# Performance work log

Hardware: AMD Instinct MI355X
Metric: run time of the kernel (lower is better)

The kernel has to match this reference:

```python
import jax, jax.numpy as jnp
import numpy as np

HEADS = 8
DK = 64   # key_size (defaults to size_per_head)
DV = 64   # size_per_head
RATE = 4
OUT = HEADS * DV  # 512


def extract_seq_patches(x, kernel, rate):
    # x: [b, L, d] -> [b, L, kernel, d]; strided local window gather
    b, L, d = x.shape
    k_size = kernel + (rate - 1) * (kernel - 1)
    p_right = (k_size - 1) // 2
    p_left = k_size - 1 - p_right
    xp = jnp.pad(x, ((0, 0), (p_left, p_right), (0, 0)))
    patches = [xp[:, i:i + L] for i in range(0, k_size, rate)]  # kernel slices
    return jnp.stack(patches, axis=2)


def setup_inputs() -> dict:
    key = jax.random.key(0)
    k1, k2, k3, k4 = jax.random.split(key, 4)
    s = 1.0 / np.sqrt(OUT)
    x = jax.random.normal(k1, (2, 4096, OUT), dtype=jnp.float32)
    Wq = jax.random.normal(k2, (OUT, HEADS * DK), dtype=jnp.float32) * s
    Wk = jax.random.normal(k3, (OUT, HEADS * DK), dtype=jnp.float32) * s
    Wv = jax.random.normal(k4, (OUT, HEADS * DV), dtype=jnp.float32) * s
    return {"x": x, "Wq": Wq, "Wk": Wk, "Wv": Wv}


def reference(x, Wq, Wk, Wv):
    b, L, d = x.shape
    pad = RATE - L % RATE  # torch code always pads (pad=RATE when L % RATE == 0)
    xpad = jnp.pad(x, ((0, 0), (0, pad), (0, 0)))
    nL = L + pad
    n = nL // RATE
    kernel = 2 * RATE - 1  # 1 + 2*neighbors

    qw = xpad @ Wq
    kw = xpad @ Wk
    vw = xpad @ Wv

    kwp = extract_seq_patches(kw, kernel, RATE)  # [b, nL, K, H*dk]
    vwp = extract_seq_patches(vw, kernel, RATE)  # [b, nL, K, H*dv]

    # [b, h, r, n, d]
    qw = qw.reshape(b, n, RATE, HEADS, DK).transpose(0, 3, 2, 1, 4)
    kw = kw.reshape(b, n, RATE, HEADS, DK).transpose(0, 3, 2, 1, 4)
    vw = vw.reshape(b, n, RATE, HEADS, DV).transpose(0, 3, 2, 1, 4)
    # [b, h, r, n, K, d]
    kwp = kwp.reshape(b, n, RATE, kernel, HEADS, DK).transpose(0, 4, 2, 1, 3, 5)
    vwp = vwp.reshape(b, n, RATE, kernel, HEADS, DV).transpose(0, 4, 2, 1, 3, 5)

    scale = 1.0 / np.sqrt(DK)
    a = jnp.einsum('bhrnd,bhrmd->bhrnm', qw, kw) * scale    # strided scores [b,h,r,n,n]
    ap = jnp.einsum('bhrnd,bhrnkd->bhrnk', qw, kwp) * scale  # local scores  [b,h,r,n,K]

    A = jax.nn.softmax(jnp.concatenate([a, ap], axis=-1), axis=-1)
    a, ap = A[..., :n], A[..., n:]

    o = jnp.einsum('bhrnm,bhrmd->bhrnd', a, vw) + jnp.einsum('bhrnk,bhrnkd->bhrnd', ap, vwp)
    o = o.transpose(0, 3, 2, 1, 4).reshape(b, nL, HEADS * DV)
    return o[:, :L]
```

## Files before the change

### kernel.cpp

```cpp
#include <hip/hip_runtime.h>
#include <hip/hip_bf16.h>


#define BATCH 2
#define LSEQ  4096
#define DMODEL 512
#define NH    8
#define DHEAD 64
#define NPAD  1088
#define QSCALE 0.18033688011112042f

typedef __bf16 bf16x8 __attribute__((ext_vector_type(8)));
typedef __attribute__((ext_vector_type(4))) float f32x4;
typedef __attribute__((ext_vector_type(16))) float f32x16;
typedef unsigned short u16;
typedef unsigned int u32;
typedef __attribute__((ext_vector_type(8))) u16 u16x8;
typedef __attribute__((ext_vector_type(4))) u16 u16x4;
typedef __attribute__((ext_vector_type(4))) u32 u32x4;

__device__ __forceinline__ u16 f2bf(float f) {
    u32 u = __float_as_uint(f);
    u += 0x7fffu + ((u >> 16) & 1u);
    return (u16)(u >> 16);
}

__device__ __forceinline__ u32 cvtpk(float lo, float hi) {
    u32 d;
    asm("v_cvt_pk_bf16_f32 %0, %1, %2" : "=v"(d) : "v"(lo), "v"(hi));
    return d;
}

__device__ __forceinline__ void gload16(const u16* g, u16* l) {
    __builtin_amdgcn_global_load_lds(
        (const __attribute__((address_space(1))) u32*)(const void*)g,
        (__attribute__((address_space(3))) u32*)(void*)l, 16, 0, 0);
}

__device__ __forceinline__ f32x16 zero16() {
    f32x16 v;
    #pragma unroll
    for (int i = 0; i < 16; ++i) v[i] = 0.f;
    return v;
}

__global__ __launch_bounds__(256) void prep_kernel(
    const float* __restrict__ x,
    const float* __restrict__ Wq, const float* __restrict__ Wk, const float* __restrict__ Wv,
    u16* __restrict__ xb, u16* __restrict__ Wt)
{
    const int bid = blockIdx.x, tid = threadIdx.x;
    if (bid < 2048) {
        const size_t i0 = (size_t)bid * 2048 + (size_t)tid * 8;
        float4 a = *(const float4*)(x + i0);
        float4 b = *(const float4*)(x + i0 + 4);
        u16x8 o = { f2bf(a.x), f2bf(a.y), f2bf(a.z), f2bf(a.w),
                    f2bf(b.x), f2bf(b.y), f2bf(b.z), f2bf(b.w) };
        *(u16x8*)(xb + i0) = o;
    } else {
        const int wb  = bid - 2048;
        const int mat = wb >> 6;
        const int t   = wb & 63;
        const int k0  = (t >> 3) * 64, c0 = (t & 7) * 64;
        const float* W = (mat == 0) ? Wq : (mat == 1) ? Wk : Wv;
        __shared__ u16 Ws[64][72];
        #pragma unroll
        for (int i = 0; i < 4; ++i) {
            const int chunk = i * 256 + tid;
            const int kr = chunk >> 4, c4 = (chunk & 15) * 4;
            float4 v = *(const float4*)(W + (size_t)(k0 + kr) * DMODEL + c0 + c4);
            u16x4 q = { f2bf(v.x), f2bf(v.y), f2bf(v.z), f2bf(v.w) };
            *(u16x4*)&Ws[kr][c4] = q;
        }
        __syncthreads();
        const int cc = tid >> 2, kq = (tid & 3) * 16;
        alignas(16) u16 tmp[16];
        #pragma unroll
        for (int kk = 0; kk < 16; ++kk) tmp[kk] = Ws[kq + kk][cc];
        u16* dst = Wt + (size_t)(mat * 512 + c0 + cc) * DMODEL + k0 + kq;
        *(u16x8*)dst       = *(const u16x8*)&tmp[0];
        *(u16x8*)(dst + 8) = *(const u16x8*)&tmp[8];
    }
}

__global__ __launch_bounds__(256) void gemm_kernel(
    const u16* __restrict__ xb, const u16* __restrict__ Wt,
    u16* __restrict__ Qb, u16* __restrict__ Kb, u16* __restrict__ Vb)
{
    const int bid = blockIdx.x;
    const int xcd = bid & 7;
    const int j   = bid >> 3;
    const int mt  = xcd * 8 + (j / 12);
    const int nt  = j % 12;
    const int m0 = mt * 128;
    const int n0 = nt * 128;
    const int tid = threadIdx.x;
    const int w = tid >> 6, l = tid & 63, lr = l & 15, lh = l >> 4;
    const int wr = w >> 1, wc = w & 1;

    __shared__ u16 smem[16896];
    u16* As = smem;
    u16* Bs = smem + 8192;

    f32x4 acc[4][4];
    const f32x4 fzero = {0.f, 0.f, 0.f, 0.f};
    #pragma unroll
    for (int mi = 0; mi < 4; ++mi)
        #pragma unroll
        for (int nj = 0; nj < 4; ++nj) acc[mi][nj] = fzero;

    for (int kt = 0; kt < 8; ++kt) {
        const int k0 = kt * 64;
        #pragma unroll
        for (int i = 0; i < 4; ++i) {
            const int cid = i * 256 + tid;
            const int row = cid >> 3, ch = cid & 7;
            const int sch = ch ^ (row & 7);
            u16* dstA = As + (i * 256 + w * 64) * 8;
            u16* dstB = Bs + (i * 256 + w * 64) * 8;
            gload16(xb + (size_t)(m0 + row) * DMODEL + k0 + sch * 8, dstA);
            gload16(Wt + (size_t)(n0 + row) * DMODEL + k0 + sch * 8, dstB);
        }
        __syncthreads();

        #pragma unroll
        for (int kk = 0; kk < 2; ++kk) {
            const int cs = (kk * 4 + lh) ^ (lr & 7);
            bf16x8 af[4], bfr[4];
            #pragma unroll
            for (int mi = 0; mi < 4; ++mi)
                af[mi] = *(const bf16x8*)(As + (wr * 64 + mi * 16 + lr) * 64 + cs * 8);
            #pragma unroll
            for (int nj = 0; nj < 4; ++nj)
                bfr[nj] = *(const bf16x8*)(Bs + (wc * 64 + nj * 16 + lr) * 64 + cs * 8);
            #pragma unroll
            for (int mi = 0; mi < 4; ++mi)
                #pragma unroll
                for (int nj = 0; nj < 4; ++nj)
                    acc[mi][nj] = __builtin_amdgcn_mfma_f32_16x16x32_bf16(af[mi], bfr[nj], acc[mi][nj], 0, 0, 0);
        }
        __syncthreads();
    }

    const int mat = nt >> 2;
    const int hp  = nt & 3;
    if (mat < 2) {
        u16* Ob = (mat == 0) ? Qb : Kb;
        const float osc = (mat == 0) ? QSCALE : 1.0f;
        #pragma unroll
        for (int mi = 0; mi < 4; ++mi) {
            const int gmb = m0 + wr * 64 + mi * 16 + lh * 4;
            const int b = gmb >> 12;
            #pragma unroll
            for (int rr = 0; rr < 4; ++rr) {
                const int t = (gmb + rr) & 4095;
                const int n = t >> 2, r = t & 3;
                #pragma unroll
                for (int nj = 0; nj < 4; ++nj) {
                    const int c  = wc * 64 + nj * 16 + lr;
                    const int h  = hp * 2 + (c >> 6);
                    const int dk = c & 63;
                    const size_t g = ((size_t)(b * NH + h)) * 4 + r;
                    Ob[(g * NPAD + n) * DHEAD + dk] = f2bf(acc[mi][nj][rr] * osc);
                }
            }
        }
    } else {
        #pragma unroll
        for (int mi = 0; mi < 4; ++mi) {
            const int nrel = wr * 16 + mi * 4 + lh;
            #pragma unroll
            for (int nj = 0; nj < 4; ++nj) {
                const int c = wc * 64 + nj * 16 + lr;
                #pragma unroll
                for (int rr = 0; rr < 4; ++rr)
                    smem[c * 132 + rr * 32 + nrel] = f2bf(acc[mi][nj][rr]);
            }
        }
        __syncthreads();
        const int b  = m0 >> 12;
        const int nb = (m0 & 4095) >> 2;
        #pragma unroll
        for (int e = 0; e < 2; ++e) {
            const int chunk = e * 256 + tid;
            const int c = chunk & 127, r = chunk >> 7;
            const int h  = hp * 2 + (c >> 6);
            const int dv = c & 63;
            const size_t g = ((size_t)(b * NH + h)) * 4 + r;
            u16* dst = Vb + (g * DHEAD + dv) * NPAD + nb;
            const u16* src = smem + c * 132 + r * 32;
            alignas(16) u16 tmp[32];
            #pragma unroll
            for (int q8 = 0; q8 < 8; ++q8)
                *(u16x4*)&tmp[q8 * 4] = *(const u16x4*)(src + q8 * 4);
            #pragma unroll
            for (int q16 = 0; q16 < 4; ++q16)
                *(u16x8*)(dst + q16 * 8) = *(const u16x8*)&tmp[q16 * 8];
        }
    }
}

__global__ __launch_bounds__(512, 4) void attn_kernel(
    const u16* __restrict__ Qb, const u16* __restrict__ Kb, const u16* __restrict__ Vb,
    float* __restrict__ out)
{
    const int g  = blockIdx.x;
    const int b  = g >> 5;
    const int h  = (g >> 2) & 7;
    const int r  = g & 3;
    const int q0 = blockIdx.y * 128;
    const int tid = threadIdx.x;
    const int w  = tid >> 6;
    const int wq = w & 3;
    const int kh = w >> 2;
    const int l  = tid & 63;
    const int lr = l & 31;
    const int hi = l >> 5;

    const u16* Qg  = Qb + (size_t)g * NPAD * DHEAD;
    const u16* Kg  = Kb + (size_t)g * NPAD * DHEAD;
    const u16* Vtg = Vb + (size_t)g * DHEAD * NPAD;

    __shared__ __align__(16) u16 KV[2][2][2][4096];
    float* red  = (float*)&KV[0][0][0][0];
    float* redL = red + 4 * 64 * 33;

    const int srow = tid >> 3;
    const int ssch = (tid & 7) ^ (srow & 7);
    const u16* ksrc0 = Kg  + (size_t)srow * DHEAD + ssch * 8;
    const u16* vsrc0 = Vtg + (size_t)srow * NPAD  + ssch * 8;

    bf16x8 qa[4];
    {
        const u16* qrow = Qg + (size_t)(q0 + wq * 32 + lr) * DHEAD + hi * 8;
        qa[0] = *(const bf16x8*)(qrow);
        qa[1] = *(const bf16x8*)(qrow + 16);
        qa[2] = *(const bf16x8*)(qrow + 32);
        qa[3] = *(const bf16x8*)(qrow + 48);
    }

    f32x16 o0 = zero16(), o1 = zero16();
    float Lown = 0.f;
    const int qw0 = q0 + wq * 32;
    const int qg  = qw0 + lr;

    gload16(ksrc0,                      &KV[0][0][0][w * 512]);
    gload16(ksrc0 + (size_t)512 * DHEAD, &KV[0][1][0][w * 512]);
    gload16(vsrc0,                      &KV[0][0][1][w * 512]);
    gload16(vsrc0 + 512,                &KV[0][1][1][w * 512]);

    for (int mt = 0; mt < 8; ++mt) {
        const int cur = mt & 1;
        if (mt < 7) {
            const size_t ko = (size_t)(mt + 1) * 64 * DHEAD;
            const int    vo = (mt + 1) * 64;
            gload16(ksrc0 + ko,                       &KV[cur ^ 1][0][0][w * 512]);
            gload16(ksrc0 + ko + (size_t)512 * DHEAD, &KV[cur ^ 1][1][0][w * 512]);
            gload16(vsrc0 + vo,                       &KV[cur ^ 1][0][1][w * 512]);
            gload16(vsrc0 + vo + 512,                 &KV[cur ^ 1][1][1][w * 512]);
            asm volatile("s_waitcnt vmcnt(4)" ::: "memory");
        } else {
            asm volatile("s_waitcnt vmcnt(0)" ::: "memory");
        }
        __builtin_amdgcn_s_barrier();

        const u16* Kbuf = &KV[cur][kh][0][0];
        const u16* Vbuf = &KV[cur][kh][1][0];

        f32x16 sA = zero16(), sB = zero16();
        __builtin_amdgcn_s_setprio(1);
        #pragma unroll
        for (int c = 0; c < 4; ++c) {
            const int slot = (c * 2 + hi) ^ (lr & 7);
            bf16x8 kbA = *(const bf16x8*)(Kbuf + (lr * 8 + slot) * 8);
            bf16x8 kbB = *(const bf16x8*)(Kbuf + ((32 + lr) * 8 + slot) * 8);
            sA = __builtin_amdgcn_mfma_f32_32x32x16_bf16(kbA, qa[c], sA, 0, 0, 0);
            sB = __builtin_amdgcn_mfma_f32_32x32x16_bf16(kbB, qa[c], sB, 0, 0, 0);
        }
        __builtin_amdgcn_s_setprio(0);

        const int mabs = kh * 512 + mt * 64;
        const bool special = (mabs + 66 >= qw0) && (mabs <= qw0 + 34);
        if (!special) {
            #pragma unroll
            for (int reg = 0; reg < 16; ++reg) {
                sA[reg] = __builtin_amdgcn_exp2f(sA[reg]);
                sB[reg] = __builtin_amdgcn_exp2f(sB[reg]);
                Lown += sA[reg] + sB[reg];
            }
        } else {
            #pragma unroll
            for (int reg = 0; reg < 16; ++reg) {
                const int krel = (reg & 3) + 8 * (reg >> 2) + 4 * hi;
                {
                    const int dd = mabs + krel - qg;
                    float v = sA[reg];
                    if (dd >= -3 && dd <= 3) v += 1.0f;
                    sA[reg] = __builtin_amdgcn_exp2f(v);
                }
                {
                    const int dd = mabs + 32 + krel - qg;
                    float v = sB[reg];
                    if (dd >= -3 && dd <= 3) v += 1.0f;
                    sB[reg] = __builtin_amdgcn_exp2f(v);
                }
                Lown += sA[reg] + sB[reg];
            }
        }

        u32 pkA[8], pkB[8];
        #pragma unroll
        for (int r2 = 0; r2 < 8; ++r2) {
            pkA[r2] = cvtpk(sA[2 * r2], sA[2 * r2 + 1]);
            pkB[r2] = cvtpk(sB[2 * r2], sB[2 * r2 + 1]);
        }

        __builtin_amdgcn_s_setprio(1);
        #pragma unroll
        for (int c = 0; c < 4; ++c) {
            const int c1 = c & 1;
            u32 p0, p1, p2, p3;
            if (c < 2) { p0 = pkA[4*c1]; p1 = pkA[4*c1+1]; p2 = pkA[4*c1+2]; p3 = pkA[4*c1+3]; }
            else       { p0 = pkB[4*c1]; p1 = pkB[4*c1+1]; p2 = pkB[4*c1+2]; p3 = pkB[4*c1+3]; }
            const u32 own0  = hi ? p2 : p0;
            const u32 own1  = hi ? p3 : p1;
            const u32 send0 = hi ? p0 : p2;
            const u32 send1 = hi ? p1 : p3;
            const u32 recv0 = (u32)__shfl_xor((int)send0, 32);
            const u32 recv1 = (u32)__shfl_xor((int)send1, 32);
            u32x4 paw;
            paw.x = hi ? recv0 : own0;
            paw.y = hi ? recv1 : own1;
            paw.z = hi ? own0  : recv0;
            paw.w = hi ? own1  : recv1;
            const bf16x8 pa = __builtin_bit_cast(bf16x8, paw);

            const int slot = (c * 2 + hi) ^ (lr & 7);
            bf16x8 vb0 = *(const bf16x8*)(Vbuf + (lr * 8 + slot) * 8);
            bf16x8 vb1 = *(const bf16x8*)(Vbuf + ((32 + lr) * 8 + slot) * 8);
            o0 = __builtin_amdgcn_mfma_f32_32x32x16_bf16(pa, vb0, o0, 0, 0, 0);
            o1 = __builtin_amdgcn_mfma_f32_32x32x16_bf16(pa, vb1, o1, 0, 0, 0);
        }
        __builtin_amdgcn_s_setprio(0);
        if (mt < 7) __syncthreads();
    }

    __syncthreads();
    if (kh == 1) {
        float* dst = red + ((size_t)wq * 64 + l) * 33;
        #pragma unroll
        for (int reg = 0; reg < 16; ++reg) {
            dst[reg]      = o0[reg];
            dst[16 + reg] = o1[reg];
        }
        redL[wq * 64 + l] = Lown;
    }
    __syncthreads();
    if (kh == 0) {
        const float* src = red + ((size_t)wq * 64 + l) * 33;
        #pragma unroll
        for (int reg = 0; reg < 16; ++reg) {
            o0[reg] += src[reg];
            o1[reg] += src[16 + reg];
        }
        Lown += redL[wq * 64 + l];

        const float Ltot = Lown + __shfl_xor(Lown, 32);
        const int coob = (qg < 3 ? 3 - qg : 0) + (qg > 1021 ? qg - 1021 : 0);
        const float inv = 1.0f / (Ltot + (float)(coob + 1 + (qg >= 1021 ? 1 : 0)));

        float iv[16];
        #pragma unroll
        for (int reg = 0; reg < 16; ++reg)
            iv[reg] = __shfl(inv, (reg & 3) + 8 * (reg >> 2) + 4 * hi);

        #pragma unroll
        for (int reg = 0; reg < 16; ++reg) {
            const int qrel = (reg & 3) + 8 * (reg >> 2) + 4 * hi;
            const int t = (q0 + wq * 32 + qrel) * 4 + r;
            float* orow = out + ((size_t)b * LSEQ + t) * DMODEL + h * DHEAD;
            orow[lr]      = o0[reg] * iv[reg];
            orow[32 + lr] = o1[reg] * iv[reg];
        }
    }
}

extern "C" void kernel_launch(void* const* d_in, const int* in_sizes, int n_in,
                              void* d_out, int out_size, void* d_ws, size_t ws_size,
                              hipStream_t stream) {
    const float* x  = (const float*)d_in[0];
    const float* Wq = (const float*)d_in[1];
    const float* Wk = (const float*)d_in[2];
    const float* Wv = (const float*)d_in[3];
    float* out = (float*)d_out;

    const size_t SZ = (size_t)BATCH * NH * 4 * NPAD * DHEAD;
    u16* Qb = (u16*)d_ws;
    u16* Kb = Qb + SZ;
    u16* Vb = Kb + SZ;

    u16* xb = (u16*)d_out;
    u16* Wt = xb + (size_t)8192 * 512;

    prep_kernel<<<2240, 256, 0, stream>>>(x, Wq, Wk, Wv, xb, Wt);

    gemm_kernel<<<768, 256, 0, stream>>>(xb, Wt, Qb, Kb, Vb);

    dim3 ga(64, 8);
    attn_kernel<<<ga, 512, 0, stream>>>(Qb, Kb, Vb, out);
}
```

Measured before the change: 69.19 us.

## Load K/V tiles directly from global memory instead of LDS double buffering

```diff
diff --git a/kernel.cpp b/kernel.cpp
--- a/kernel.cpp
+++ b/kernel.cpp
@@ -221,14 +221,8 @@
     const u16* Kg  = Kb + (size_t)g * NPAD * DHEAD;
     const u16* Vtg = Vb + (size_t)g * DHEAD * NPAD;
 
-    __shared__ __align__(16) u16 KV[2][2][2][4096];
-    float* red  = (float*)&KV[0][0][0][0];
-    float* redL = red + 4 * 64 * 33;
-
-    const int srow = tid >> 3;
-    const int ssch = (tid & 7) ^ (srow & 7);
-    const u16* ksrc0 = Kg  + (size_t)srow * DHEAD + ssch * 8;
-    const u16* vsrc0 = Vtg + (size_t)srow * NPAD  + ssch * 8;
+    __shared__ float red[4 * 64 * 33];
+    __shared__ float redL[4 * 64];
 
     bf16x8 qa[4];
     {
@@ -244,42 +238,23 @@
     const int qw0 = q0 + wq * 32;
     const int qg  = qw0 + lr;
 
-    gload16(ksrc0,                      &KV[0][0][0][w * 512]);
-    gload16(ksrc0 + (size_t)512 * DHEAD, &KV[0][1][0][w * 512]);
-    gload16(vsrc0,                      &KV[0][0][1][w * 512]);
-    gload16(vsrc0 + 512,                &KV[0][1][1][w * 512]);
-
     for (int mt = 0; mt < 8; ++mt) {
-        const int cur = mt & 1;
-        if (mt < 7) {
-            const size_t ko = (size_t)(mt + 1) * 64 * DHEAD;
-            const int    vo = (mt + 1) * 64;
-            gload16(ksrc0 + ko,                       &KV[cur ^ 1][0][0][w * 512]);
-            gload16(ksrc0 + ko + (size_t)512 * DHEAD, &KV[cur ^ 1][1][0][w * 512]);
-            gload16(vsrc0 + vo,                       &KV[cur ^ 1][0][1][w * 512]);
-            gload16(vsrc0 + vo + 512,                 &KV[cur ^ 1][1][1][w * 512]);
-            asm volatile("s_waitcnt vmcnt(4)" ::: "memory");
-        } else {
-            asm volatile("s_waitcnt vmcnt(0)" ::: "memory");
-        }
-        __builtin_amdgcn_s_barrier();
-
-        const u16* Kbuf = &KV[cur][kh][0][0];
-        const u16* Vbuf = &KV[cur][kh][1][0];
+        const int mabs = kh * 512 + mt * 64;
+        const u16* Kt = Kg  + (size_t)mabs * DHEAD;
+        const u16* Vt = Vtg + mabs;
 
         f32x16 sA = zero16(), sB = zero16();
         __builtin_amdgcn_s_setprio(1);
         #pragma unroll
         for (int c = 0; c < 4; ++c) {
-            const int slot = (c * 2 + hi) ^ (lr & 7);
-            bf16x8 kbA = *(const bf16x8*)(Kbuf + (lr * 8 + slot) * 8);
-            bf16x8 kbB = *(const bf16x8*)(Kbuf + ((32 + lr) * 8 + slot) * 8);
+            const int ch = c * 2 + hi;
+            bf16x8 kbA = *(const bf16x8*)(Kt + (size_t)lr * DHEAD + ch * 8);
+            bf16x8 kbB = *(const bf16x8*)(Kt + (size_t)(32 + lr) * DHEAD + ch * 8);
             sA = __builtin_amdgcn_mfma_f32_32x32x16_bf16(kbA, qa[c], sA, 0, 0, 0);
             sB = __builtin_amdgcn_mfma_f32_32x32x16_bf16(kbB, qa[c], sB, 0, 0, 0);
         }
         __builtin_amdgcn_s_setprio(0);
 
-        const int mabs = kh * 512 + mt * 64;
         const bool special = (mabs + 66 >= qw0) && (mabs <= qw0 + 34);
         if (!special) {
             #pragma unroll
@@ -335,17 +310,15 @@
             paw.w = hi ? own1  : recv1;
             const bf16x8 pa = __builtin_bit_cast(bf16x8, paw);
 
-            const int slot = (c * 2 + hi) ^ (lr & 7);
-            bf16x8 vb0 = *(const bf16x8*)(Vbuf + (lr * 8 + slot) * 8);
-            bf16x8 vb1 = *(const bf16x8*)(Vbuf + ((32 + lr) * 8 + slot) * 8);
+            const int ch = c * 2 + hi;
+            bf16x8 vb0 = *(const bf16x8*)(Vt + (size_t)lr * NPAD + ch * 8);
+            bf16x8 vb1 = *(const bf16x8*)(Vt + (size_t)(32 + lr) * NPAD + ch * 8);
             o0 = __builtin_amdgcn_mfma_f32_32x32x16_bf16(pa, vb0, o0, 0, 0, 0);
             o1 = __builtin_amdgcn_mfma_f32_32x32x16_bf16(pa, vb1, o1, 0, 0, 0);
         }
         __builtin_amdgcn_s_setprio(0);
-        if (mt < 7) __syncthreads();
-    }
-
-    __syncthreads();
+    }
+
     if (kh == 1) {
         float* dst = red + ((size_t)wq * 64 + l) * 33;
         #pragma unroll
```

New measurement: 99.34 us. 43.6% more time.
